# Kernel optimization log

Hardware: AMD Instinct MI355X
Metric: run time of the kernel (lower is better)

Reference implementation:

```python
import jax, jax.numpy as jnp
import numpy as np

N_HEADS = 16


def setup_inputs() -> dict:
    key = jax.random.key(0)
    ks = jax.random.split(key, 10)
    B, M, N, C, D = 2, 2048, 2048, 1024, 1024
    s = 0.02
    return {
        "kv": jax.random.normal(ks[0], (B, M, C), jnp.float32),
        "q": jax.random.normal(ks[1], (B, N, D), jnp.float32),
        "Wk": jax.random.normal(ks[2], (C, D), jnp.float32) * s,
        "bk": jnp.zeros((D,), jnp.float32),
        "Wq": jax.random.normal(ks[3], (D, D), jnp.float32) * s,
        "bq": jnp.zeros((D,), jnp.float32),
        "Wv": jax.random.normal(ks[4], (C, D), jnp.float32) * s,
        "bv": jnp.zeros((D,), jnp.float32),
        "Wp": jax.random.normal(ks[5], (D, D), jnp.float32) * s,
        "bp": jnp.zeros((D,), jnp.float32),
    }


def reference(kv, q, Wk, bk, Wq, bq, Wv, bv, Wp, bp):
    B, M, C = kv.shape
    B2, N, D = q.shape
    H = N_HEADS
    hd = D // H
    # projections (weights stored as [in, out]; torch Linear is x @ W.T + b with W [out,in])
    k = (kv @ Wk + bk).reshape(B, M, H, hd).transpose(0, 2, 1, 3)  # [B,H,M,hd]
    qh = (q @ Wq + bq).reshape(B, N, H, hd).transpose(0, 2, 1, 3)  # [B,H,N,hd]
    v = (kv @ Wv + bv).reshape(B, M, H, hd).transpose(0, 2, 1, 3)  # [B,H,M,hd]
    scale = 1.0 / jnp.sqrt(jnp.asarray(hd, k.dtype))
    att = jnp.einsum("bhnd,bhmd->bhnm", qh, k) * scale
    att = jax.nn.softmax(att, axis=-1)
    y = jnp.einsum("bhnm,bhmd->bhnd", att, v)  # [B,H,N,hd]
    y = y.transpose(0, 2, 1, 3).reshape(B, N, D)
    return y @ Wp + bp
```

## Files before the change

kernel.cpp:

```cpp
#include <hip/hip_runtime.h>

#define DV 1024
#define HD 64

typedef short v4s __attribute__((ext_vector_type(4)));
typedef short v8s __attribute__((ext_vector_type(8)));
typedef float v4f __attribute__((ext_vector_type(4)));
typedef int   v2i __attribute__((ext_vector_type(2)));

__device__ __forceinline__ short f2bf(float x){
  unsigned u = __float_as_uint(x);
  u += 0x7FFFu + ((u >> 16) & 1u);
  return (short)(u >> 16);
}

__device__ __forceinline__ int swz(int lane){
  return (((lane & 7) ^ (lane >> 3)) << 3);
}

__global__ __launch_bounds__(256) void cvt2(const float* __restrict__ xa,
                                            const float* __restrict__ xb,
                                            short* __restrict__ ya,
                                            short* __restrict__ yb, int n){
  const float* x = blockIdx.y ? xb : xa;
  short* y = blockIdx.y ? yb : ya;
  int stride = gridDim.x * 256 * 4;
  for (int i = (blockIdx.x * 256 + threadIdx.x) * 4; i < n; i += stride){
    float4 v = *(const float4*)(x + i);
    v4s s; s.x = f2bf(v.x); s.y = f2bf(v.y); s.z = f2bf(v.z); s.w = f2bf(v.w);
    *(v4s*)(y + i) = s;
  }
}

__global__ __launch_bounds__(256) void tcvt4(
    const float* __restrict__ W0, const float* __restrict__ W1,
    const float* __restrict__ W2, const float* __restrict__ W3,
    short* __restrict__ T0, short* __restrict__ T1,
    short* __restrict__ T2, short* __restrict__ T3){
  const float* W; short* Wt;
  switch (blockIdx.z){
    case 0: W = W0; Wt = T0; break;
    case 1: W = W1; Wt = T1; break;
    case 2: W = W2; Wt = T2; break;
    default: W = W3; Wt = T3; break;
  }
  __shared__ short L[64 * 68];
  const int t = threadIdx.x;
  const int k0 = blockIdx.y * 64, n0 = blockIdx.x * 64;
  const int rr = t >> 4, cc = (t & 15) * 4;
  #pragma unroll
  for (int j = 0; j < 4; j++){
    int r = rr + j * 16;
    float4 v = *(const float4*)(W + (size_t)(k0 + r) * DV + n0 + cc);
    v4s s; s.x = f2bf(v.x); s.y = f2bf(v.y); s.z = f2bf(v.z); s.w = f2bf(v.w);
    *(v4s*)&L[r * 68 + cc] = s;
  }
  __syncthreads();
  #pragma unroll
  for (int j = 0; j < 4; j++){
    int n = rr + j * 16;
    v4s s;
    s.x = L[(cc + 0) * 68 + n];
    s.y = L[(cc + 1) * 68 + n];
    s.z = L[(cc + 2) * 68 + n];
    s.w = L[(cc + 3) * 68 + n];
    *(v4s*)(Wt + (size_t)(n0 + n) * DV + k0 + cc) = s;
  }
}

template<typename OUT_T>
__device__ __forceinline__ void gemm_tile(
    const short* __restrict__ A, const short* __restrict__ Bt,
    const float* __restrict__ bias, OUT_T* __restrict__ C,
    int M, int N, int K, float out_scale, int m0, int n0, bool bias_row)
{
  __shared__ short As[128 * 64];
  __shared__ short Bs[128 * 64];
  const int tid = threadIdx.x;
  const int wave = tid >> 6, lane = tid & 63;
  const int quad = lane >> 4, l15 = lane & 15;
  const int wr = (wave >> 1) * 64, wc = (wave & 1) * 64;
  const int srow = lane >> 3;
  const int sw = swz(lane);
  const v4f vzero = {0.f, 0.f, 0.f, 0.f};

  const short* pa[4]; const short* pb[4];
  #pragma unroll
  for (int ii = 0; ii < 4; ii++){
    int i = wave * 4 + ii;
    pa[ii] = A  + (size_t)(m0 + i * 8 + srow) * K + sw;
    pb[ii] = Bt + (size_t)(n0 + i * 8 + srow) * K + sw;
  }

  v8s ra[4], rb[4];
  #pragma unroll
  for (int ii = 0; ii < 4; ii++){
    ra[ii] = *(const v8s*)(pa[ii]);
    rb[ii] = *(const v8s*)(pb[ii]);
  }

  v4f acc[4][4];
  #pragma unroll
  for (int i = 0; i < 4; i++)
    #pragma unroll
    for (int j = 0; j < 4; j++)
      acc[i][j] = vzero;

  for (int kt = 0; kt < K; kt += 64){
    __syncthreads();
    #pragma unroll
    for (int ii = 0; ii < 4; ii++){
      int i = wave * 4 + ii;
      *(v8s*)&As[i * 512 + lane * 8] = ra[ii];
      *(v8s*)&Bs[i * 512 + lane * 8] = rb[ii];
    }
    __syncthreads();
    if (kt + 64 < K){
      #pragma unroll
      for (int ii = 0; ii < 4; ii++){
        ra[ii] = *(const v8s*)(pa[ii] + kt + 64);
        rb[ii] = *(const v8s*)(pb[ii] + kt + 64);
      }
    }
    #pragma unroll
    for (int ks = 0; ks < 2; ks++){
      v8s a[4], b[4];
      #pragma unroll
      for (int mt = 0; mt < 4; mt++)
        a[mt] = *(const v8s*)&As[(wr + mt * 16 + l15) * 64 + (((ks * 4 + quad) ^ (l15 & 7)) << 3)];
      #pragma unroll
      for (int nt = 0; nt < 4; nt++)
        b[nt] = *(const v8s*)&Bs[(wc + nt * 16 + l15) * 64 + (((ks * 4 + quad) ^ (l15 & 7)) << 3)];
      #pragma unroll
      for (int mt = 0; mt < 4; mt++)
        #pragma unroll
        for (int nt = 0; nt < 4; nt++)
          acc[mt][nt] = __builtin_amdgcn_mfma_f32_16x16x32_bf16(a[mt], b[nt], acc[mt][nt], 0, 0, 0);
    }
  }

  #pragma unroll
  for (int mt = 0; mt < 4; mt++){
    #pragma unroll
    for (int nt = 0; nt < 4; nt++){
      int row = m0 + wr + mt * 16 + quad * 4;
      int col = n0 + wc + nt * 16 + l15;
      float bcol = bias_row ? 0.0f : bias[col];
      #pragma unroll
      for (int r = 0; r < 4; r++){
        float bv = bias_row ? bias[row + r] : bcol;
        float v = (acc[mt][nt][r] + bv) * out_scale;
        if (sizeof(OUT_T) == 2)
          ((short*)C)[(size_t)(row + r) * N + col] = f2bf(v);
        else
          ((float*)C)[(size_t)(row + r) * N + col] = v;
      }
    }
  }
}

__global__ __launch_bounds__(256, 3) void proj3(
    const short* __restrict__ qb, const short* __restrict__ kvb,
    const short* __restrict__ Wqt, const short* __restrict__ Wkt,
    const short* __restrict__ Wvt,
    const float* __restrict__ bq, const float* __restrict__ bk,
    const float* __restrict__ bv,
    short* __restrict__ Qp, short* __restrict__ Kp, short* __restrict__ VT,
    float qscale)
{
  int bid = blockIdx.x;
  const short *A, *Bt; const float* bias; short* C;
  int M, N, m0, n0; float scale; bool brow;
  if (bid < 512){
    int z = bid >> 8, l = bid & 255;
    M = 4096; N = 1024; m0 = (l & 31) * 128; n0 = (l >> 5) * 128;
    A = z ? kvb : qb; Bt = z ? Wkt : Wqt; bias = z ? bk : bq;
    C = z ? Kp : Qp; scale = z ? 1.0f : qscale; brow = false;
  } else {
    int l = bid - 512;
    M = 1024; N = 4096; m0 = (l >> 5) * 128; n0 = (l & 31) * 128;
    A = Wvt; Bt = kvb; bias = bv; C = VT; scale = 1.0f; brow = true;
  }
  gemm_tile<short>(A, Bt, bias, C, M, N, 1024, scale, m0, n0, brow);
}

__global__ __launch_bounds__(256, 2) void gemm_f32(
    const short* __restrict__ A, const short* __restrict__ Bt,
    const float* __restrict__ bias, float* __restrict__ C)
{
  __shared__ short As[128 * 64];
  __shared__ short Bs[64 * 64];
  const int tid = threadIdx.x;
  const int wave = tid >> 6, lane = tid & 63;
  const int quad = lane >> 4, l15 = lane & 15;
  const int bid = blockIdx.x;
  const int m0 = (bid & 31) * 128, n0 = (bid >> 5) * 64;
  const int wr = (wave >> 1) * 64, wc = (wave & 1) * 32;
  const int srow = lane >> 3;
  const int sw = swz(lane);
  const int K = 1024;
  const v4f vzero = {0.f, 0.f, 0.f, 0.f};

  const short* pa[4]; const short* pb[2];
  #pragma unroll
  for (int ii = 0; ii < 4; ii++)
    pa[ii] = A + (size_t)(m0 + (wave * 4 + ii) * 8 + srow) * K + sw;
  #pragma unroll
  for (int ii = 0; ii < 2; ii++)
    pb[ii] = Bt + (size_t)(n0 + (wave * 2 + ii) * 8 + srow) * K + sw;

  v8s ra[4], rb[2];
  #pragma unroll
  for (int ii = 0; ii < 4; ii++) ra[ii] = *(const v8s*)(pa[ii]);
  #pragma unroll
  for (int ii = 0; ii < 2; ii++) rb[ii] = *(const v8s*)(pb[ii]);

  v4f acc[4][2];
  #pragma unroll
  for (int i = 0; i < 4; i++){ acc[i][0] = vzero; acc[i][1] = vzero; }

  for (int kt = 0; kt < K; kt += 64){
    __syncthreads();
    #pragma unroll
    for (int ii = 0; ii < 4; ii++)
      *(v8s*)&As[(wave * 4 + ii) * 512 + lane * 8] = ra[ii];
    #pragma unroll
    for (int ii = 0; ii < 2; ii++)
      *(v8s*)&Bs[(wave * 2 + ii) * 512 + lane * 8] = rb[ii];
    __syncthreads();
    if (kt + 64 < K){
      #pragma unroll
      for (int ii = 0; ii < 4; ii++) ra[ii] = *(const v8s*)(pa[ii] + kt + 64);
      #pragma unroll
      for (int ii = 0; ii < 2; ii++) rb[ii] = *(const v8s*)(pb[ii] + kt + 64);
    }
    #pragma unroll
    for (int ks = 0; ks < 2; ks++){
      v8s a[4], b[2];
      #pragma unroll
      for (int mt = 0; mt < 4; mt++)
        a[mt] = *(const v8s*)&As[(wr + mt * 16 + l15) * 64 + (((ks * 4 + quad) ^ (l15 & 7)) << 3)];
      #pragma unroll
      for (int nt = 0; nt < 2; nt++)
        b[nt] = *(const v8s*)&Bs[(wc + nt * 16 + l15) * 64 + (((ks * 4 + quad) ^ (l15 & 7)) << 3)];
      #pragma unroll
      for (int mt = 0; mt < 4; mt++)
        #pragma unroll
        for (int nt = 0; nt < 2; nt++)
          acc[mt][nt] = __builtin_amdgcn_mfma_f32_16x16x32_bf16(a[mt], b[nt], acc[mt][nt], 0, 0, 0);
    }
  }

  #pragma unroll
  for (int mt = 0; mt < 4; mt++){
    #pragma unroll
    for (int nt = 0; nt < 2; nt++){
      int row = m0 + wr + mt * 16 + quad * 4;
      int col = n0 + wc + nt * 16 + l15;
      float bcol = bias[col];
      #pragma unroll
      for (int r = 0; r < 4; r++)
        C[(size_t)(row + r) * 1024 + col] = acc[mt][nt][r] + bcol;
    }
  }
}

__global__ __launch_bounds__(256, 3) void attn(
    const short* __restrict__ Qp, const short* __restrict__ Kp,
    const short* __restrict__ Vt, short* __restrict__ Y)
{
  __shared__ short Ks[64 * 64];
  __shared__ short Vs[64 * 68];
  const int tid = threadIdx.x;
  const int wave = tid >> 6, lane = tid & 63;
  const int quad = lane >> 4, l15 = lane & 15;
  const int gid = blockIdx.x;
  const int qi = gid >> 5, bh = gid & 31;
  const int h = bh & 15, b = bh >> 4;
  const int n0 = qi * 128;
  const int srow = lane >> 3;
  const int c8 = (lane & 7) * 8;
  const int sw = swz(lane);
  const size_t rowbase = (size_t)b * 2048;
  const v4f vzero = {0.f, 0.f, 0.f, 0.f};

  v8s qf[2][2];
  #pragma unroll
  for (int qt = 0; qt < 2; qt++){
    const short* qrow = Qp + (rowbase + n0 + wave * 32 + qt * 16 + l15) * DV + h * HD + quad * 8;
    qf[qt][0] = *(const v8s*)(qrow);
    qf[qt][1] = *(const v8s*)(qrow + 32);
  }

  const short* pk[2]; const short* pv[2];
  #pragma unroll
  for (int ii = 0; ii < 2; ii++){
    int i = wave * 2 + ii;
    pk[ii] = Kp + (rowbase + i * 8 + srow) * DV + h * HD + sw;
    pv[ii] = Vt + (size_t)(h * HD + i * 8 + srow) * 4096 + rowbase + c8;
  }
  v8s rk[2], rv[2];
  #pragma unroll
  for (int ii = 0; ii < 2; ii++){ rk[ii] = *(const v8s*)(pk[ii]); rv[ii] = *(const v8s*)(pv[ii]); }

  v4f o[4][2];
  #pragma unroll
  for (int dt = 0; dt < 4; dt++){ o[dt][0] = vzero; o[dt][1] = vzero; }
  float lsum[2] = {0.0f, 0.0f};

  for (int kt = 0; kt < 32; kt++){
    __syncthreads();
    #pragma unroll
    for (int ii = 0; ii < 2; ii++){
      int i = wave * 2 + ii;
      *(v8s*)&Ks[i * 512 + lane * 8] = rk[ii];
      *(v8s*)&Vs[(i * 8 + srow) * 68 + c8] = rv[ii];
    }
    __syncthreads();
    if (kt < 31){
      #pragma unroll
      for (int ii = 0; ii < 2; ii++){
        rk[ii] = *(const v8s*)(pk[ii] + (size_t)(kt + 1) * 64 * DV);
        rv[ii] = *(const v8s*)(pv[ii] + (kt + 1) * 64);
      }
    }

    v4f s[2][4];
    #pragma unroll
    for (int qt = 0; qt < 2; qt++)
      #pragma unroll
      for (int kvt = 0; kvt < 4; kvt++) s[qt][kvt] = vzero;
    #pragma unroll
    for (int ks = 0; ks < 2; ks++){
      v8s a[4];
      #pragma unroll
      for (int kvt = 0; kvt < 4; kvt++)
        a[kvt] = *(const v8s*)&Ks[(kvt * 16 + l15) * 64 + (((ks * 4 + quad) ^ (l15 & 7)) << 3)];
      #pragma unroll
      for (int kvt = 0; kvt < 4; kvt++)
        #pragma unroll
        for (int qt = 0; qt < 2; qt++)
          s[qt][kvt] = __builtin_amdgcn_mfma_f32_16x16x32_bf16(a[kvt], qf[qt][ks], s[qt][kvt], 0, 0, 0);
    }

    v4s pf[2][4];
    #pragma unroll
    for (int qt = 0; qt < 2; qt++)
      #pragma unroll
      for (int kvt = 0; kvt < 4; kvt++){
        float p0 = __builtin_amdgcn_exp2f(s[qt][kvt][0]);
        float p1 = __builtin_amdgcn_exp2f(s[qt][kvt][1]);
        float p2 = __builtin_amdgcn_exp2f(s[qt][kvt][2]);
        float p3 = __builtin_amdgcn_exp2f(s[qt][kvt][3]);
        lsum[qt] += (p0 + p1) + (p2 + p3);
        unsigned u0 = __float_as_uint(p0) + 0x8000u;
        unsigned u1 = __float_as_uint(p1) + 0x8000u;
        unsigned u2 = __float_as_uint(p2) + 0x8000u;
        unsigned u3 = __float_as_uint(p3) + 0x8000u;
        v2i pi;
        pi.x = (int)__builtin_amdgcn_perm(u1, u0, 0x07060302u);
        pi.y = (int)__builtin_amdgcn_perm(u3, u2, 0x07060302u);
        pf[qt][kvt] = __builtin_bit_cast(v4s, pi);
      }

    #pragma unroll
    for (int ks = 0; ks < 4; ks++){
      v4s a[4];
      #pragma unroll
      for (int dt = 0; dt < 4; dt++)
        a[dt] = *(const v4s*)&Vs[(dt * 16 + l15) * 68 + ks * 16 + quad * 4];
      #pragma unroll
      for (int dt = 0; dt < 4; dt++)
        #pragma unroll
        for (int qt = 0; qt < 2; qt++)
          o[dt][qt] = __builtin_amdgcn_mfma_f32_16x16x16bf16_1k(a[dt], pf[qt][ks], o[dt][qt], 0, 0, 0);
    }
  }

  #pragma unroll
  for (int qt = 0; qt < 2; qt++){
    float ls = lsum[qt];
    ls += __shfl_xor(ls, 16);
    ls += __shfl_xor(ls, 32);
    float inv = 1.0f / ls;
    size_t row = rowbase + n0 + wave * 32 + qt * 16 + l15;
    #pragma unroll
    for (int dt = 0; dt < 4; dt++){
      int col = h * HD + dt * 16 + quad * 4;
      unsigned p0 = (unsigned short)f2bf(o[dt][qt][0] * inv) |
                    ((unsigned)(unsigned short)f2bf(o[dt][qt][1] * inv) << 16);
      unsigned p1 = (unsigned short)f2bf(o[dt][qt][2] * inv) |
                    ((unsigned)(unsigned short)f2bf(o[dt][qt][3] * inv) << 16);
      *(unsigned*)(Y + row * DV + col)     = p0;
      *(unsigned*)(Y + row * DV + col + 2) = p1;
    }
  }
}

extern "C" void kernel_launch(void* const* d_in, const int* in_sizes, int n_in,
                              void* d_out, int out_size, void* d_ws, size_t ws_size,
                              hipStream_t stream) {
  const float* kv = (const float*)d_in[0];
  const float* q  = (const float*)d_in[1];
  const float* Wk = (const float*)d_in[2];
  const float* bk = (const float*)d_in[3];
  const float* Wq = (const float*)d_in[4];
  const float* bq = (const float*)d_in[5];
  const float* Wv = (const float*)d_in[6];
  const float* bv = (const float*)d_in[7];
  const float* Wp = (const float*)d_in[8];
  const float* bp = (const float*)d_in[9];

  const size_t E  = 4194304;
  const size_t WE = 1048576;
  short* p   = (short*)d_ws;
  short* kvb = p; p += E;
  short* qb  = p; p += E;
  short* Wkt = p; p += WE;
  short* Wqt = p; p += WE;
  short* Wvt = p; p += WE;
  short* Wpt = p; p += WE;
  short* Kp  = p; p += E;
  short* Qp  = p; p += E;
  short* VT  = p; p += E;
  short* Yb  = p; p += E;

  cvt2<<<dim3(512, 2), 256, 0, stream>>>(kv, q, kvb, qb, (int)E);
  tcvt4<<<dim3(16, 16, 4), 256, 0, stream>>>(Wk, Wq, Wv, Wp, Wkt, Wqt, Wvt, Wpt);

  proj3<<<768, 256, 0, stream>>>(qb, kvb, Wqt, Wkt, Wvt, bq, bk, bv,
                                 Qp, Kp, VT, 0.18033688011f);

  attn<<<512, 256, 0, stream>>>(Qp, Kp, VT, Yb);

  gemm_f32<<<512, 256, 0, stream>>>(Yb, Wpt, bp, (float*)d_out);
}
```

Baseline: 206.2 us.

## Fuse all stages into one persistent kernel with atomic grid barriers

Replaces five separate kernel launches (conversion, weight transpose, projections, attention, output GEMM) with one persistent 768-block kernel that separates the stages with software grid barriers built on atomic counters. The aim is to remove launch gaps and per-kernel tail effects between stages. In exchange every stage runs at the same block count and occupancy (launch bounds 3). The barrier also assumes all 768 blocks are resident at the same time, and it would deadlock if they were not. The attention and output GEMM stages leave 256 blocks idle, and a memset is added for the barrier counters.

```diff
diff --git a/kernel.cpp b/kernel.cpp
--- a/kernel.cpp
+++ b/kernel.cpp
@@ -18,64 +18,24 @@
   return (((lane & 7) ^ (lane >> 3)) << 3);
 }
 
-__global__ __launch_bounds__(256) void cvt2(const float* __restrict__ xa,
-                                            const float* __restrict__ xb,
-                                            short* __restrict__ ya,
-                                            short* __restrict__ yb, int n){
-  const float* x = blockIdx.y ? xb : xa;
-  short* y = blockIdx.y ? yb : ya;
-  int stride = gridDim.x * 256 * 4;
-  for (int i = (blockIdx.x * 256 + threadIdx.x) * 4; i < n; i += stride){
-    float4 v = *(const float4*)(x + i);
-    v4s s; s.x = f2bf(v.x); s.y = f2bf(v.y); s.z = f2bf(v.z); s.w = f2bf(v.w);
-    *(v4s*)(y + i) = s;
-  }
-}
-
-__global__ __launch_bounds__(256) void tcvt4(
-    const float* __restrict__ W0, const float* __restrict__ W1,
-    const float* __restrict__ W2, const float* __restrict__ W3,
-    short* __restrict__ T0, short* __restrict__ T1,
-    short* __restrict__ T2, short* __restrict__ T3){
-  const float* W; short* Wt;
-  switch (blockIdx.z){
-    case 0: W = W0; Wt = T0; break;
-    case 1: W = W1; Wt = T1; break;
-    case 2: W = W2; Wt = T2; break;
-    default: W = W3; Wt = T3; break;
-  }
-  __shared__ short L[64 * 68];
-  const int t = threadIdx.x;
-  const int k0 = blockIdx.y * 64, n0 = blockIdx.x * 64;
-  const int rr = t >> 4, cc = (t & 15) * 4;
-  #pragma unroll
-  for (int j = 0; j < 4; j++){
-    int r = rr + j * 16;
-    float4 v = *(const float4*)(W + (size_t)(k0 + r) * DV + n0 + cc);
-    v4s s; s.x = f2bf(v.x); s.y = f2bf(v.y); s.z = f2bf(v.z); s.w = f2bf(v.w);
-    *(v4s*)&L[r * 68 + cc] = s;
-  }
+__device__ __forceinline__ void gridbar(unsigned* ctr, unsigned target){
   __syncthreads();
-  #pragma unroll
-  for (int j = 0; j < 4; j++){
-    int n = rr + j * 16;
-    v4s s;
-    s.x = L[(cc + 0) * 68 + n];
-    s.y = L[(cc + 1) * 68 + n];
-    s.z = L[(cc + 2) * 68 + n];
-    s.w = L[(cc + 3) * 68 + n];
-    *(v4s*)(Wt + (size_t)(n0 + n) * DV + k0 + cc) = s;
-  }
-}
-
-template<typename OUT_T>
-__device__ __forceinline__ void gemm_tile(
+  if (threadIdx.x == 0){
+    __hip_atomic_fetch_add(ctr, 1u, __ATOMIC_RELEASE, __HIP_MEMORY_SCOPE_AGENT);
+    while (__hip_atomic_load(ctr, __ATOMIC_RELAXED, __HIP_MEMORY_SCOPE_AGENT) < target)
+      __builtin_amdgcn_s_sleep(8);
+    __threadfence();
+  }
+  __syncthreads();
+}
+
+__device__ void gemm_tile_sm(short* SM,
     const short* __restrict__ A, const short* __restrict__ Bt,
-    const float* __restrict__ bias, OUT_T* __restrict__ C,
-    int M, int N, int K, float out_scale, int m0, int n0, bool bias_row)
+    const float* __restrict__ bias, short* __restrict__ C,
+    int N, int K, float out_scale, int m0, int n0, bool bias_row)
 {
-  __shared__ short As[128 * 64];
-  __shared__ short Bs[128 * 64];
+  short* As = SM;
+  short* Bs = SM + 8192;
   const int tid = threadIdx.x;
   const int wave = tid >> 6, lane = tid & 63;
   const int quad = lane >> 4, l15 = lane & 15;
@@ -149,250 +109,291 @@
       #pragma unroll
       for (int r = 0; r < 4; r++){
         float bv = bias_row ? bias[row + r] : bcol;
-        float v = (acc[mt][nt][r] + bv) * out_scale;
-        if (sizeof(OUT_T) == 2)
-          ((short*)C)[(size_t)(row + r) * N + col] = f2bf(v);
-        else
-          ((float*)C)[(size_t)(row + r) * N + col] = v;
-      }
-    }
-  }
-}
-
-__global__ __launch_bounds__(256, 3) void proj3(
-    const short* __restrict__ qb, const short* __restrict__ kvb,
-    const short* __restrict__ Wqt, const short* __restrict__ Wkt,
-    const short* __restrict__ Wvt,
-    const float* __restrict__ bq, const float* __restrict__ bk,
-    const float* __restrict__ bv,
-    short* __restrict__ Qp, short* __restrict__ Kp, short* __restrict__ VT,
-    float qscale)
+        C[(size_t)(row + r) * N + col] = f2bf((acc[mt][nt][r] + bv) * out_scale);
+      }
+    }
+  }
+}
+
+__global__ __launch_bounds__(256, 3) void mega(
+    const float* __restrict__ kv, const float* __restrict__ q,
+    const float* __restrict__ Wk, const float* __restrict__ bk,
+    const float* __restrict__ Wq, const float* __restrict__ bq,
+    const float* __restrict__ Wv, const float* __restrict__ bv,
+    const float* __restrict__ Wp, const float* __restrict__ bp,
+    short* __restrict__ kvb, short* __restrict__ qb,
+    short* __restrict__ Wkt, short* __restrict__ Wqt,
+    short* __restrict__ Wvt, short* __restrict__ Wpt,
+    short* __restrict__ Kp, short* __restrict__ Qp,
+    short* __restrict__ VT, short* __restrict__ Yb,
+    float* __restrict__ out, unsigned* __restrict__ bar, float qscale)
 {
-  int bid = blockIdx.x;
-  const short *A, *Bt; const float* bias; short* C;
-  int M, N, m0, n0; float scale; bool brow;
+  __shared__ short SM[16384];
+  const int bid = blockIdx.x;
+  const int tid = threadIdx.x;
+
+  {
+    const int stride = 768 * 256 * 4;
+    for (int i = (bid * 256 + tid) * 4; i < 4194304; i += stride){
+      float4 v = *(const float4*)(kv + i);
+      v4s s; s.x = f2bf(v.x); s.y = f2bf(v.y); s.z = f2bf(v.z); s.w = f2bf(v.w);
+      *(v4s*)(kvb + i) = s;
+      float4 w = *(const float4*)(q + i);
+      v4s u; u.x = f2bf(w.x); u.y = f2bf(w.y); u.z = f2bf(w.z); u.w = f2bf(w.w);
+      *(v4s*)(qb + i) = u;
+    }
+    const int rr = tid >> 4, cc = (tid & 15) * 4;
+    for (int uu = bid; uu < 1024; uu += 768){
+      const float* W; short* Wt;
+      switch (uu >> 8){
+        case 0: W = Wk; Wt = Wkt; break;
+        case 1: W = Wq; Wt = Wqt; break;
+        case 2: W = Wv; Wt = Wvt; break;
+        default: W = Wp; Wt = Wpt; break;
+      }
+      const int tl = uu & 255;
+      const int k0 = (tl >> 4) * 64, n0 = (tl & 15) * 64;
+      __syncthreads();
+      #pragma unroll
+      for (int j = 0; j < 4; j++){
+        int r = rr + j * 16;
+        float4 v = *(const float4*)(W + (size_t)(k0 + r) * DV + n0 + cc);
+        v4s s; s.x = f2bf(v.x); s.y = f2bf(v.y); s.z = f2bf(v.z); s.w = f2bf(v.w);
+        *(v4s*)&SM[r * 68 + cc] = s;
+      }
+      __syncthreads();
+      #pragma unroll
+      for (int j = 0; j < 4; j++){
+        int n = rr + j * 16;
+        v4s s;
+        s.x = SM[(cc + 0) * 68 + n];
+        s.y = SM[(cc + 1) * 68 + n];
+        s.z = SM[(cc + 2) * 68 + n];
+        s.w = SM[(cc + 3) * 68 + n];
+        *(v4s*)(Wt + (size_t)(n0 + n) * DV + k0 + cc) = s;
+      }
+    }
+  }
+  gridbar(bar + 0, 768);
+
+  {
+    const short *A, *Bt2; const float* bias; short* C;
+    int N, m0, n0; float scale; bool brow;
+    if (bid < 512){
+      int z = bid >> 8, l = bid & 255;
+      N = 1024; m0 = (l & 31) * 128; n0 = (l >> 5) * 128;
+      A = z ? kvb : qb; Bt2 = z ? Wkt : Wqt; bias = z ? bk : bq;
+      C = z ? Kp : Qp; scale = z ? 1.0f : qscale; brow = false;
+    } else {
+      int l = bid - 512;
+      N = 4096; m0 = (l >> 5) * 128; n0 = (l & 31) * 128;
+      A = Wvt; Bt2 = kvb; bias = bv; C = VT; scale = 1.0f; brow = true;
+    }
+    gemm_tile_sm(SM, A, Bt2, bias, C, N, 1024, scale, m0, n0, brow);
+  }
+  gridbar(bar + 1, 768);
+
   if (bid < 512){
-    int z = bid >> 8, l = bid & 255;
-    M = 4096; N = 1024; m0 = (l & 31) * 128; n0 = (l >> 5) * 128;
-    A = z ? kvb : qb; Bt = z ? Wkt : Wqt; bias = z ? bk : bq;
-    C = z ? Kp : Qp; scale = z ? 1.0f : qscale; brow = false;
-  } else {
-    int l = bid - 512;
-    M = 1024; N = 4096; m0 = (l >> 5) * 128; n0 = (l & 31) * 128;
-    A = Wvt; Bt = kvb; bias = bv; C = VT; scale = 1.0f; brow = true;
-  }
-  gemm_tile<short>(A, Bt, bias, C, M, N, 1024, scale, m0, n0, brow);
-}
-
-__global__ __launch_bounds__(256, 2) void gemm_f32(
-    const short* __restrict__ A, const short* __restrict__ Bt,
-    const float* __restrict__ bias, float* __restrict__ C)
-{
-  __shared__ short As[128 * 64];
-  __shared__ short Bs[64 * 64];
-  const int tid = threadIdx.x;
-  const int wave = tid >> 6, lane = tid & 63;
-  const int quad = lane >> 4, l15 = lane & 15;
-  const int bid = blockIdx.x;
-  const int m0 = (bid & 31) * 128, n0 = (bid >> 5) * 64;
-  const int wr = (wave >> 1) * 64, wc = (wave & 1) * 32;
-  const int srow = lane >> 3;
-  const int sw = swz(lane);
-  const int K = 1024;
-  const v4f vzero = {0.f, 0.f, 0.f, 0.f};
-
-  const short* pa[4]; const short* pb[2];
-  #pragma unroll
-  for (int ii = 0; ii < 4; ii++)
-    pa[ii] = A + (size_t)(m0 + (wave * 4 + ii) * 8 + srow) * K + sw;
-  #pragma unroll
-  for (int ii = 0; ii < 2; ii++)
-    pb[ii] = Bt + (size_t)(n0 + (wave * 2 + ii) * 8 + srow) * K + sw;
-
-  v8s ra[4], rb[2];
-  #pragma unroll
-  for (int ii = 0; ii < 4; ii++) ra[ii] = *(const v8s*)(pa[ii]);
-  #pragma unroll
-  for (int ii = 0; ii < 2; ii++) rb[ii] = *(const v8s*)(pb[ii]);
-
-  v4f acc[4][2];
-  #pragma unroll
-  for (int i = 0; i < 4; i++){ acc[i][0] = vzero; acc[i][1] = vzero; }
-
-  for (int kt = 0; kt < K; kt += 64){
-    __syncthreads();
-    #pragma unroll
-    for (int ii = 0; ii < 4; ii++)
-      *(v8s*)&As[(wave * 4 + ii) * 512 + lane * 8] = ra[ii];
-    #pragma unroll
-    for (int ii = 0; ii < 2; ii++)
-      *(v8s*)&Bs[(wave * 2 + ii) * 512 + lane * 8] = rb[ii];
-    __syncthreads();
-    if (kt + 64 < K){
-      #pragma unroll
-      for (int ii = 0; ii < 4; ii++) ra[ii] = *(const v8s*)(pa[ii] + kt + 64);
-      #pragma unroll
-      for (int ii = 0; ii < 2; ii++) rb[ii] = *(const v8s*)(pb[ii] + kt + 64);
-    }
-    #pragma unroll
-    for (int ks = 0; ks < 2; ks++){
-      v8s a[4], b[2];
-      #pragma unroll
-      for (int mt = 0; mt < 4; mt++)
-        a[mt] = *(const v8s*)&As[(wr + mt * 16 + l15) * 64 + (((ks * 4 + quad) ^ (l15 & 7)) << 3)];
-      #pragma unroll
-      for (int nt = 0; nt < 2; nt++)
-        b[nt] = *(const v8s*)&Bs[(wc + nt * 16 + l15) * 64 + (((ks * 4 + quad) ^ (l15 & 7)) << 3)];
-      #pragma unroll
-      for (int mt = 0; mt < 4; mt++)
-        #pragma unroll
-        for (int nt = 0; nt < 2; nt++)
-          acc[mt][nt] = __builtin_amdgcn_mfma_f32_16x16x32_bf16(a[mt], b[nt], acc[mt][nt], 0, 0, 0);
-    }
-  }
-
-  #pragma unroll
-  for (int mt = 0; mt < 4; mt++){
-    #pragma unroll
-    for (int nt = 0; nt < 2; nt++){
-      int row = m0 + wr + mt * 16 + quad * 4;
-      int col = n0 + wc + nt * 16 + l15;
-      float bcol = bias[col];
-      #pragma unroll
-      for (int r = 0; r < 4; r++)
-        C[(size_t)(row + r) * 1024 + col] = acc[mt][nt][r] + bcol;
-    }
-  }
-}
-
-__global__ __launch_bounds__(256, 3) void attn(
-    const short* __restrict__ Qp, const short* __restrict__ Kp,
-    const short* __restrict__ Vt, short* __restrict__ Y)
-{
-  __shared__ short Ks[64 * 64];
-  __shared__ short Vs[64 * 68];
-  const int tid = threadIdx.x;
-  const int wave = tid >> 6, lane = tid & 63;
-  const int quad = lane >> 4, l15 = lane & 15;
-  const int gid = blockIdx.x;
-  const int qi = gid >> 5, bh = gid & 31;
-  const int h = bh & 15, b = bh >> 4;
-  const int n0 = qi * 128;
-  const int srow = lane >> 3;
-  const int c8 = (lane & 7) * 8;
-  const int sw = swz(lane);
-  const size_t rowbase = (size_t)b * 2048;
-  const v4f vzero = {0.f, 0.f, 0.f, 0.f};
-
-  v8s qf[2][2];
-  #pragma unroll
-  for (int qt = 0; qt < 2; qt++){
-    const short* qrow = Qp + (rowbase + n0 + wave * 32 + qt * 16 + l15) * DV + h * HD + quad * 8;
-    qf[qt][0] = *(const v8s*)(qrow);
-    qf[qt][1] = *(const v8s*)(qrow + 32);
-  }
-
-  const short* pk[2]; const short* pv[2];
-  #pragma unroll
-  for (int ii = 0; ii < 2; ii++){
-    int i = wave * 2 + ii;
-    pk[ii] = Kp + (rowbase + i * 8 + srow) * DV + h * HD + sw;
-    pv[ii] = Vt + (size_t)(h * HD + i * 8 + srow) * 4096 + rowbase + c8;
-  }
-  v8s rk[2], rv[2];
-  #pragma unroll
-  for (int ii = 0; ii < 2; ii++){ rk[ii] = *(const v8s*)(pk[ii]); rv[ii] = *(const v8s*)(pv[ii]); }
-
-  v4f o[4][2];
-  #pragma unroll
-  for (int dt = 0; dt < 4; dt++){ o[dt][0] = vzero; o[dt][1] = vzero; }
-  float lsum[2] = {0.0f, 0.0f};
-
-  for (int kt = 0; kt < 32; kt++){
-    __syncthreads();
+    short* Ks = SM;
+    short* Vs = SM + 4096;
+    const int wave = tid >> 6, lane = tid & 63;
+    const int quad = lane >> 4, l15 = lane & 15;
+    const int qi = bid >> 5, bh = bid & 31;
+    const int h = bh & 15, b = bh >> 4;
+    const int n0 = qi * 128;
+    const int srow = lane >> 3;
+    const int c8 = (lane & 7) * 8;
+    const int sw = swz(lane);
+    const size_t rowbase = (size_t)b * 2048;
+    const v4f vzero = {0.f, 0.f, 0.f, 0.f};
+
+    v8s qf[2][2];
+    #pragma unroll
+    for (int qt = 0; qt < 2; qt++){
+      const short* qrow = Qp + (rowbase + n0 + wave * 32 + qt * 16 + l15) * DV + h * HD + quad * 8;
+      qf[qt][0] = *(const v8s*)(qrow);
+      qf[qt][1] = *(const v8s*)(qrow + 32);
+    }
+
+    const short* pk[2]; const short* pv[2];
     #pragma unroll
     for (int ii = 0; ii < 2; ii++){
       int i = wave * 2 + ii;
-      *(v8s*)&Ks[i * 512 + lane * 8] = rk[ii];
-      *(v8s*)&Vs[(i * 8 + srow) * 68 + c8] = rv[ii];
-    }
-    __syncthreads();
-    if (kt < 31){
+      pk[ii] = Kp + (rowbase + i * 8 + srow) * DV + h * HD + sw;
+      pv[ii] = VT + (size_t)(h * HD + i * 8 + srow) * 4096 + rowbase + c8;
+    }
+    v8s rk[2], rv[2];
+    #pragma unroll
+    for (int ii = 0; ii < 2; ii++){ rk[ii] = *(const v8s*)(pk[ii]); rv[ii] = *(const v8s*)(pv[ii]); }
+
+    v4f o[4][2];
+    #pragma unroll
+    for (int dt = 0; dt < 4; dt++){ o[dt][0] = vzero; o[dt][1] = vzero; }
+    float lsum[2] = {0.0f, 0.0f};
+
+    for (int kt = 0; kt < 32; kt++){
+      __syncthreads();
       #pragma unroll
       for (int ii = 0; ii < 2; ii++){
-        rk[ii] = *(const v8s*)(pk[ii] + (size_t)(kt + 1) * 64 * DV);
-        rv[ii] = *(const v8s*)(pv[ii] + (kt + 1) * 64);
-      }
-    }
-
-    v4f s[2][4];
-    #pragma unroll
-    for (int qt = 0; qt < 2; qt++)
-      #pragma unroll
-      for (int kvt = 0; kvt < 4; kvt++) s[qt][kvt] = vzero;
-    #pragma unroll
-    for (int ks = 0; ks < 2; ks++){
-      v8s a[4];
-      #pragma unroll
-      for (int kvt = 0; kvt < 4; kvt++)
-        a[kvt] = *(const v8s*)&Ks[(kvt * 16 + l15) * 64 + (((ks * 4 + quad) ^ (l15 & 7)) << 3)];
-      #pragma unroll
-      for (int kvt = 0; kvt < 4; kvt++)
-        #pragma unroll
-        for (int qt = 0; qt < 2; qt++)
-          s[qt][kvt] = __builtin_amdgcn_mfma_f32_16x16x32_bf16(a[kvt], qf[qt][ks], s[qt][kvt], 0, 0, 0);
-    }
-
-    v4s pf[2][4];
-    #pragma unroll
-    for (int qt = 0; qt < 2; qt++)
-      #pragma unroll
-      for (int kvt = 0; kvt < 4; kvt++){
-        float p0 = __builtin_amdgcn_exp2f(s[qt][kvt][0]);
-        float p1 = __builtin_amdgcn_exp2f(s[qt][kvt][1]);
-        float p2 = __builtin_amdgcn_exp2f(s[qt][kvt][2]);
-        float p3 = __builtin_amdgcn_exp2f(s[qt][kvt][3]);
-        lsum[qt] += (p0 + p1) + (p2 + p3);
-        unsigned u0 = __float_as_uint(p0) + 0x8000u;
-        unsigned u1 = __float_as_uint(p1) + 0x8000u;
-        unsigned u2 = __float_as_uint(p2) + 0x8000u;
-        unsigned u3 = __float_as_uint(p3) + 0x8000u;
-        v2i pi;
-        pi.x = (int)__builtin_amdgcn_perm(u1, u0, 0x07060302u);
-        pi.y = (int)__builtin_amdgcn_perm(u3, u2, 0x07060302u);
-        pf[qt][kvt] = __builtin_bit_cast(v4s, pi);
-      }
-
-    #pragma unroll
-    for (int ks = 0; ks < 4; ks++){
-      v4s a[4];
-      #pragma unroll
-      for (int dt = 0; dt < 4; dt++)
-        a[dt] = *(const v4s*)&Vs[(dt * 16 + l15) * 68 + ks * 16 + quad * 4];
-      #pragma unroll
-      for (int dt = 0; dt < 4; dt++)
-        #pragma unroll
-        for (int qt = 0; qt < 2; qt++)
-          o[dt][qt] = __builtin_amdgcn_mfma_f32_16x16x16bf16_1k(a[dt], pf[qt][ks], o[dt][qt], 0, 0, 0);
-    }
-  }
-
-  #pragma unroll
-  for (int qt = 0; qt < 2; qt++){
-    float ls = lsum[qt];
-    ls += __shfl_xor(ls, 16);
-    ls += __shfl_xor(ls, 32);
-    float inv = 1.0f / ls;
-    size_t row = rowbase + n0 + wave * 32 + qt * 16 + l15;
-    #pragma unroll
-    for (int dt = 0; dt < 4; dt++){
-      int col = h * HD + dt * 16 + quad * 4;
-      unsigned p0 = (unsigned short)f2bf(o[dt][qt][0] * inv) |
-                    ((unsigned)(unsigned short)f2bf(o[dt][qt][1] * inv) << 16);
-      unsigned p1 = (unsigned short)f2bf(o[dt][qt][2] * inv) |
-                    ((unsigned)(unsigned short)f2bf(o[dt][qt][3] * inv) << 16);
-      *(unsigned*)(Y + row * DV + col)     = p0;
-      *(unsigned*)(Y + row * DV + col + 2) = p1;
+        int i = wave * 2 + ii;
+        *(v8s*)&Ks[i * 512 + lane * 8] = rk[ii];
+        *(v8s*)&Vs[(i * 8 + srow) * 68 + c8] = rv[ii];
+      }
+      __syncthreads();
+      if (kt < 31){
+        #pragma unroll
+        for (int ii = 0; ii < 2; ii++){
+          rk[ii] = *(const v8s*)(pk[ii] + (size_t)(kt + 1) * 64 * DV);
+          rv[ii] = *(const v8s*)(pv[ii] + (kt + 1) * 64);
+        }
+      }
+
+      v4f s[2][4];
+      #pragma unroll
+      for (int qt = 0; qt < 2; qt++)
+        #pragma unroll
+        for (int kvt = 0; kvt < 4; kvt++) s[qt][kvt] = vzero;
+      #pragma unroll
+      for (int ks = 0; ks < 2; ks++){
+        v8s a[4];
+        #pragma unroll
+        for (int kvt = 0; kvt < 4; kvt++)
+          a[kvt] = *(const v8s*)&Ks[(kvt * 16 + l15) * 64 + (((ks * 4 + quad) ^ (l15 & 7)) << 3)];
+        #pragma unroll
+        for (int kvt = 0; kvt < 4; kvt++)
+          #pragma unroll
+          for (int qt = 0; qt < 2; qt++)
+            s[qt][kvt] = __builtin_amdgcn_mfma_f32_16x16x32_bf16(a[kvt], qf[qt][ks], s[qt][kvt], 0, 0, 0);
+      }
+
+      v4s pf[2][4];
+      #pragma unroll
+      for (int qt = 0; qt < 2; qt++)
+        #pragma unroll
+        for (int kvt = 0; kvt < 4; kvt++){
+          float p0 = __builtin_amdgcn_exp2f(s[qt][kvt][0]);
+          float p1 = __builtin_amdgcn_exp2f(s[qt][kvt][1]);
+          float p2 = __builtin_amdgcn_exp2f(s[qt][kvt][2]);
+          float p3 = __builtin_amdgcn_exp2f(s[qt][kvt][3]);
+          lsum[qt] += (p0 + p1) + (p2 + p3);
+          unsigned u0 = __float_as_uint(p0) + 0x8000u;
+          unsigned u1 = __float_as_uint(p1) + 0x8000u;
+          unsigned u2 = __float_as_uint(p2) + 0x8000u;
+          unsigned u3 = __float_as_uint(p3) + 0x8000u;
+          v2i pi;
+          pi.x = (int)__builtin_amdgcn_perm(u1, u0, 0x07060302u);
+          pi.y = (int)__builtin_amdgcn_perm(u3, u2, 0x07060302u);
+          pf[qt][kvt] = __builtin_bit_cast(v4s, pi);
+        }
+
+      #pragma unroll
+      for (int ks = 0; ks < 4; ks++){
+        v4s a[4];
+        #pragma unroll
+        for (int dt = 0; dt < 4; dt++)
+          a[dt] = *(const v4s*)&Vs[(dt * 16 + l15) * 68 + ks * 16 + quad * 4];
+        #pragma unroll
+        for (int dt = 0; dt < 4; dt++)
+          #pragma unroll
+          for (int qt = 0; qt < 2; qt++)
+            o[dt][qt] = __builtin_amdgcn_mfma_f32_16x16x16bf16_1k(a[dt], pf[qt][ks], o[dt][qt], 0, 0, 0);
+      }
+    }
+
+    #pragma unroll
+    for (int qt = 0; qt < 2; qt++){
+      float ls = lsum[qt];
+      ls += __shfl_xor(ls, 16);
+      ls += __shfl_xor(ls, 32);
+      float inv = 1.0f / ls;
+      size_t row = rowbase + n0 + wave * 32 + qt * 16 + l15;
+      #pragma unroll
+      for (int dt = 0; dt < 4; dt++){
+        int col = h * HD + dt * 16 + quad * 4;
+        unsigned p0 = (unsigned short)f2bf(o[dt][qt][0] * inv) |
+                      ((unsigned)(unsigned short)f2bf(o[dt][qt][1] * inv) << 16);
+        unsigned p1 = (unsigned short)f2bf(o[dt][qt][2] * inv) |
+                      ((unsigned)(unsigned short)f2bf(o[dt][qt][3] * inv) << 16);
+        *(unsigned*)(Yb + row * DV + col)     = p0;
+        *(unsigned*)(Yb + row * DV + col + 2) = p1;
+      }
+    }
+  }
+  gridbar(bar + 2, 768);
+
+  if (bid < 512){
+    short* As = SM;
+    short* Bs = SM + 8192;
+    const int wave = tid >> 6, lane = tid & 63;
+    const int quad = lane >> 4, l15 = lane & 15;
+    const int m0 = (bid & 31) * 128, n0 = (bid >> 5) * 64;
+    const int wr = (wave >> 1) * 64, wc = (wave & 1) * 32;
+    const int srow = lane >> 3;
+    const int sw = swz(lane);
+    const int K = 1024;
+    const v4f vzero = {0.f, 0.f, 0.f, 0.f};
+
+    const short* pa[4]; const short* pb[2];
+    #pragma unroll
+    for (int ii = 0; ii < 4; ii++)
+      pa[ii] = Yb + (size_t)(m0 + (wave * 4 + ii) * 8 + srow) * K + sw;
+    #pragma unroll
+    for (int ii = 0; ii < 2; ii++)
+      pb[ii] = Wpt + (size_t)(n0 + (wave * 2 + ii) * 8 + srow) * K + sw;
+
+    v8s ra[4], rb[2];
+    #pragma unroll
+    for (int ii = 0; ii < 4; ii++) ra[ii] = *(const v8s*)(pa[ii]);
+    #pragma unroll
+    for (int ii = 0; ii < 2; ii++) rb[ii] = *(const v8s*)(pb[ii]);
+
+    v4f acc[4][2];
+    #pragma unroll
+    for (int i = 0; i < 4; i++){ acc[i][0] = vzero; acc[i][1] = vzero; }
+
+    for (int kt = 0; kt < K; kt += 64){
+      __syncthreads();
+      #pragma unroll
+      for (int ii = 0; ii < 4; ii++)
+        *(v8s*)&As[(wave * 4 + ii) * 512 + lane * 8] = ra[ii];
+      #pragma unroll
+      for (int ii = 0; ii < 2; ii++)
+        *(v8s*)&Bs[(wave * 2 + ii) * 512 + lane * 8] = rb[ii];
+      __syncthreads();
+      if (kt + 64 < K){
+        #pragma unroll
+        for (int ii = 0; ii < 4; ii++) ra[ii] = *(const v8s*)(pa[ii] + kt + 64);
+        #pragma unroll
+        for (int ii = 0; ii < 2; ii++) rb[ii] = *(const v8s*)(pb[ii] + kt + 64);
+      }
+      #pragma unroll
+      for (int ks = 0; ks < 2; ks++){
+        v8s a[4], b[2];
+        #pragma unroll
+        for (int mt = 0; mt < 4; mt++)
+          a[mt] = *(const v8s*)&As[(wr + mt * 16 + l15) * 64 + (((ks * 4 + quad) ^ (l15 & 7)) << 3)];
+        #pragma unroll
+        for (int nt = 0; nt < 2; nt++)
+          b[nt] = *(const v8s*)&Bs[(wc + nt * 16 + l15) * 64 + (((ks * 4 + quad) ^ (l15 & 7)) << 3)];
+        #pragma unroll
+        for (int mt = 0; mt < 4; mt++)
+          #pragma unroll
+          for (int nt = 0; nt < 2; nt++)
+            acc[mt][nt] = __builtin_amdgcn_mfma_f32_16x16x32_bf16(a[mt], b[nt], acc[mt][nt], 0, 0, 0);
+      }
+    }
+
+    #pragma unroll
+    for (int mt = 0; mt < 4; mt++){
+      #pragma unroll
+      for (int nt = 0; nt < 2; nt++){
+        int row = m0 + wr + mt * 16 + quad * 4;
+        int col = n0 + wc + nt * 16 + l15;
+        float bcol = bp[col];
+        #pragma unroll
+        for (int r = 0; r < 4; r++)
+          out[(size_t)(row + r) * 1024 + col] = acc[mt][nt][r] + bcol;
+      }
     }
   }
 }
@@ -424,14 +425,11 @@
   short* Qp  = p; p += E;
   short* VT  = p; p += E;
   short* Yb  = p; p += E;
-
-  cvt2<<<dim3(512, 2), 256, 0, stream>>>(kv, q, kvb, qb, (int)E);
-  tcvt4<<<dim3(16, 16, 4), 256, 0, stream>>>(Wk, Wq, Wv, Wp, Wkt, Wqt, Wvt, Wpt);
-
-  proj3<<<768, 256, 0, stream>>>(qb, kvb, Wqt, Wkt, Wvt, bq, bk, bv,
-                                 Qp, Kp, VT, 0.18033688011f);
-
-  attn<<<512, 256, 0, stream>>>(Qp, Kp, VT, Yb);
-
-  gemm_f32<<<512, 256, 0, stream>>>(Yb, Wpt, bp, (float*)d_out);
-}
+  unsigned* bar = (unsigned*)p;
+
+  hipMemsetAsync(bar, 0, 256, stream);
+  mega<<<768, 256, 0, stream>>>(kv, q, Wk, bk, Wq, bq, Wv, bv, Wp, bp,
+                                kvb, qb, Wkt, Wqt, Wvt, Wpt,
+                                Kp, Qp, VT, Yb, (float*)d_out,
+                                bar, 0.18033688011f);
+}
```

Result: slower. 451.1 us (+118.7%).
